# Optimization experiments

Hardware: AMD Instinct MI355X
Metric: run time of the kernel (lower is better)

The kernel has to match this reference:

```python
import jax, jax.numpy as jnp
import numpy as np

B, S, D, H, T = 16, 512, 512, 8, 8
DK = D // H
SCALE = float(1.0 / np.sqrt(DK))
EPS = 1e-5


def setup_inputs() -> dict:
    key = jax.random.key(0)
    ks = jax.random.split(key, 12)
    s = float(1.0 / np.sqrt(D))  # torch Linear default init scale
    u = lambda k, shp: jax.random.uniform(k, shp, jnp.float32, -s, s)
    return {
        "x": jax.random.normal(ks[0], (B, S, D), jnp.float32),
        "x_type": jax.random.randint(ks[1], (B, S), 0, T, jnp.int32),
        "mask": jax.random.randint(ks[2], (B, S, S), 0, 2, jnp.int32),
        "Wq": u(ks[3], (T, D, D)), "bq": u(ks[4], (T, D)),
        "Wk": u(ks[5], (T, D, D)), "bk": u(ks[6], (T, D)),
        "Wv": u(ks[7], (T, D, D)), "bv": u(ks[8], (T, D)),
        "Wa": u(ks[9], (T, D, D)), "ba": u(ks[10], (T, D)),
        "gamma": jnp.ones((T, D), jnp.float32),
        "beta": jnp.zeros((T, D), jnp.float32),
    }


def _typed_proj(xf, t, W, b):
    # per-node-type linear 'experts': compute all T projections, select by type id
    # xf: [N, D], W: [T, D, D], b: [T, D], t: [N] -> [N, D]
    all_p = jnp.einsum('nd,tdh->nth', xf, W) + b[None]  # [N, T, D]
    return jnp.take_along_axis(all_p, t[:, None, None], axis=1)[:, 0]


def reference(x, x_type, mask, Wq, bq, Wk, bk, Wv, bv, Wa, ba, gamma, beta):
    xf = x.reshape(-1, D)          # [N, D], N = B*S
    t = x_type.reshape(-1)         # [N]

    # heterogeneous Q/K/V dispatch
    q = _typed_proj(xf, t, Wq, bq).reshape(B, S, H, DK).transpose(0, 2, 1, 3)
    k = _typed_proj(xf, t, Wk, bk).reshape(B, S, H, DK).transpose(0, 2, 1, 3)
    v = _typed_proj(xf, t, Wv, bv).reshape(B, S, H, DK).transpose(0, 2, 1, 3)

    # scaled dot-product attention with boolean mask (mask==0 -> -1e9)
    scores = jnp.einsum('bhqd,bhkd->bhqk', q, k) * SCALE  # [B, H, S, S]
    scores = jnp.where(mask[:, None] == 0, jnp.float32(-1e9), scores)
    p = jax.nn.softmax(scores, axis=-1)
    att = jnp.einsum('bhqk,bhkd->bhqd', p, v)             # [B, H, S, DK]
    att = att.transpose(0, 2, 1, 3).reshape(-1, D)        # [N, D]

    # per-type output projection + residual + per-type LayerNorm
    a = _typed_proj(att, t, Wa, ba)
    h = a + xf
    mu = jnp.mean(h, axis=-1, keepdims=True)
    var = jnp.mean((h - mu) ** 2, axis=-1, keepdims=True)
    out = (h - mu) * jax.lax.rsqrt(var + EPS) * gamma[t] + beta[t]
    return out.reshape(B, S, D)
```

## Files before the change

kernel.cpp:

```cpp
#include <hip/hip_runtime.h>
#include <hip/hip_bf16.h>

typedef __attribute__((ext_vector_type(8))) short short8;
typedef __attribute__((ext_vector_type(4))) float f32x4;
typedef __attribute__((ext_vector_type(4))) unsigned short u16x4;
typedef unsigned short u16;
typedef unsigned int u32;
typedef unsigned long long u64;

#define NB 16
#define NS 512
#define ND 512
#define NH 8
#define NT 8
#define NDK 64
#define NN (NB*NS)
#define SCALE_LOG2E 0.18033688011112042f
#define BM 128
#define BN 128
#define BKK 64

__device__ __forceinline__ u16 f2bf(float f) {
    __hip_bfloat16 h = __float2bfloat16(f);
    return *reinterpret_cast<u16*>(&h);
}
__device__ __forceinline__ u32 pk2(float lo, float hi) {
    return (u32)f2bf(lo) | ((u32)f2bf(hi) << 16);
}

typedef const __attribute__((address_space(1))) void* gas_t;
typedef __attribute__((address_space(3))) void* las_t;

__device__ __forceinline__ void gload16(const void* gsrc, void* ldst) {
    __builtin_amdgcn_global_load_lds((gas_t)gsrc, (las_t)ldst, 16, 0, 0);
}

__global__ __launch_bounds__(256) void pre_all(
    const float* __restrict__ x, const int* __restrict__ xty, const int* __restrict__ mask,
    const float* __restrict__ Wq, const float* __restrict__ Wk,
    const float* __restrict__ Wv, const float* __restrict__ Wa,
    u16* __restrict__ xb,
    u16* __restrict__ Wqt, u16* __restrict__ Wkt, u16* __restrict__ Wvt, u16* __restrict__ Wat,
    u64* __restrict__ maskb, int* __restrict__ gcnt, int* __restrict__ scnt)
{
    __shared__ __align__(16) float tile[64][68];
    __shared__ int cnt[NT];
    int bid = blockIdx.x, tid = threadIdx.x;

    if (bid < 4096) {
        int i = bid * 256 + tid;
        float4 v = reinterpret_cast<const float4*>(x)[i];
        u16x4 o;
        o.x = f2bf(v.x); o.y = f2bf(v.y); o.z = f2bf(v.z); o.w = f2bf(v.w);
        reinterpret_cast<u16x4*>(xb)[i] = o;
    } else if (bid < 6144) {
        int wid = bid - 4096;
        int bx = wid & 7, by = (wid >> 3) & 7, bz = wid >> 6;
        int arr = bz >> 3, t = bz & 7;
        const float* W = (arr == 0 ? Wq : arr == 1 ? Wk : arr == 2 ? Wv : Wa) + ((size_t)t << 18);
        u16* O = (arr == 0 ? Wqt : arr == 1 ? Wkt : arr == 2 ? Wvt : Wat) + ((size_t)t << 18);
        int d0 = bx * 64, h0 = by * 64;
        int tx = tid & 15, ty = tid >> 4;
        #pragma unroll
        for (int i = 0; i < 4; ++i) {
            int r = ty + i * 16;
            float4 v = *reinterpret_cast<const float4*>(&W[(size_t)(d0 + r) * ND + h0 + tx * 4]);
            *reinterpret_cast<float4*>(&tile[r][tx * 4]) = v;
        }
        __syncthreads();
        #pragma unroll
        for (int i = 0; i < 4; ++i) {
            int r = ty + i * 16;
            u16x4 o;
            o.x = f2bf(tile[tx * 4 + 0][r]);
            o.y = f2bf(tile[tx * 4 + 1][r]);
            o.z = f2bf(tile[tx * 4 + 2][r]);
            o.w = f2bf(tile[tx * 4 + 3][r]);
            *reinterpret_cast<u16x4*>(&O[(size_t)(h0 + r) * ND + d0 + tx * 4]) = o;
        }
    } else if (bid < 7168) {
        int base = (bid - 6144) * 16;
        #pragma unroll
        for (int c = 0; c < 16; ++c) {
            int i = (base + c) * 256 + tid;
            int v = mask[i];
            u64 bal = __ballot(v != 0);
            if ((tid & 63) == 0) maskb[i >> 6] = bal;
        }
    } else {
        int s = bid - 7168;
        if (tid < NT) cnt[tid] = 0;
        __syncthreads();
        if (tid < 128) atomicAdd(&cnt[xty[s * 128 + tid]], 1);
        __syncthreads();
        if (tid < NT) {
            scnt[s * 8 + tid] = cnt[tid];
            atomicAdd(&gcnt[tid], cnt[tid]);
        }
    }
}

__global__ __launch_bounds__(256) void scatter_k(
    const int* __restrict__ xty, const int* __restrict__ gcnt, const int* __restrict__ scnt,
    int* __restrict__ perm, int* __restrict__ typeoff,
    int* __restrict__ tile_type, int* __restrict__ tile_row0, int* __restrict__ ntiles)
{
    __shared__ int base[NT];
    int s = blockIdx.x, tid = threadIdx.x;
    if (tid < NT) {
        int off = 0;
        for (int tt = 0; tt < tid; ++tt) off += gcnt[tt];
        base[tid] = off;
    }
    __syncthreads();
    {
        int t = tid & 7;
        for (int ss = tid >> 3; ss < s; ss += 32) atomicAdd(&base[t], scnt[ss * 8 + t]);
    }
    __syncthreads();
    if (tid < 128) {
        int n = s * 128 + tid;
        int t = xty[n];
        int p = atomicAdd(&base[t], 1);
        perm[p] = n;
    }
    if (s == 0 && tid == 0) {
        int acc = 0, nt = 0;
        for (int t = 0; t < NT; ++t) {
            typeoff[t] = acc;
            int c = gcnt[t];
            for (int r = 0; r < c; r += BM) { tile_type[nt] = t; tile_row0[nt] = acc + r; ++nt; }
            acc += c;
        }
        typeoff[NT] = acc;
        *ntiles = nt;
    }
}

__global__ __launch_bounds__(256) void qkv_gemm(
    const u16* __restrict__ xb,
    const u16* __restrict__ Wqt, const u16* __restrict__ Wkt, const u16* __restrict__ Wvt,
    const float* __restrict__ bq, const float* __restrict__ bk, const float* __restrict__ bv,
    const int* __restrict__ perm, const int* __restrict__ typeoff,
    const int* __restrict__ tile_type, const int* __restrict__ tile_row0, const int* __restrict__ ntiles,
    u16* __restrict__ qb, u16* __restrict__ kbf, u16* __restrict__ vb)
{
    int work = (blockIdx.x & 7) * 108 + (blockIdx.x >> 3);
    int tile = work / 12, pc = work % 12;
    if (tile >= *ntiles) return;
    int t = tile_type[tile];
    int row0 = tile_row0[tile];
    int rows = typeoff[t + 1] - row0; if (rows > BM) rows = BM;
    int proj = pc >> 2;
    int col0 = (pc & 3) * BN;
    const u16* W = (proj == 0 ? Wqt : proj == 1 ? Wkt : Wvt) + ((size_t)t << 18);
    const float* bias = (proj == 0 ? bq : proj == 1 ? bk : bv) + (t << 9);
    u16* outp = proj == 0 ? qb : proj == 1 ? kbf : vb;
    float qscale = proj == 0 ? SCALE_LOG2E : 1.f;

    __shared__ __align__(16) u16 smem[2][2][BM][BKK];
    __shared__ int stok[BM];
    auto As = smem[0]; auto Bs = smem[1];

    int tid = threadIdx.x;
    if (tid < BM) stok[tid] = perm[row0 + (tid < rows ? tid : 0)];
    __syncthreads();

    int lane = tid & 63, w = tid >> 6;
    int wr = w >> 1, wc = w & 1;
    int fr = lane & 15, g = lane >> 4;

    int lrow = lane >> 3;
    int schunk = (lane & 7) ^ lrow;
    int tokA[4];
    #pragma unroll
    for (int k = 0; k < 4; ++k) tokA[k] = stok[w * 32 + k * 8 + lrow];

    auto stage = [&](int buf, int k0) {
        #pragma unroll
        for (int k = 0; k < 4; ++k) {
            gload16(xb + (((size_t)tokA[k]) << 9) + k0 + schunk * 8, &As[buf][w * 32 + k * 8][0]);
            gload16(W + (((size_t)(col0 + w * 32 + k * 8 + lrow)) << 9) + k0 + schunk * 8,
                    &Bs[buf][w * 32 + k * 8][0]);
        }
    };

    f32x4 acc[4][4] = {};

    stage(0, 0);
    #pragma unroll
    for (int it = 0; it < 8; ++it) {
        int cur = it & 1;
        if (it < 7) {
            stage(cur ^ 1, (it + 1) * BKK);
            asm volatile("s_waitcnt vmcnt(8)" ::: "memory");
        } else {
            asm volatile("s_waitcnt vmcnt(0)" ::: "memory");
        }
        __builtin_amdgcn_s_barrier();

        const char* Ab = (const char*)As[cur];
        const char* Bb = (const char*)Bs[cur];
        #pragma unroll
        for (int ks = 0; ks < 2; ++ks) {
            short8 af[4], bfr[4];
            #pragma unroll
            for (int m = 0; m < 4; ++m) {
                int r = wr * 64 + m * 16 + fr;
                af[m] = *reinterpret_cast<const short8*>(Ab + r * 128 + (((ks * 4 + g) ^ (r & 7)) << 4));
            }
            #pragma unroll
            for (int n = 0; n < 4; ++n) {
                int r = wc * 64 + n * 16 + fr;
                bfr[n] = *reinterpret_cast<const short8*>(Bb + r * 128 + (((ks * 4 + g) ^ (r & 7)) << 4));
            }
            #pragma unroll
            for (int m = 0; m < 4; ++m)
                #pragma unroll
                for (int n = 0; n < 4; ++n)
                    acc[m][n] = __builtin_amdgcn_mfma_f32_16x16x32_bf16(af[m], bfr[n], acc[m][n], 0, 0, 0);
        }
        asm volatile("s_waitcnt lgkmcnt(0)" ::: "memory");
        __builtin_amdgcn_s_barrier();
    }

    u16 (*sT)[136] = reinterpret_cast<u16 (*)[136]>(&smem[0][0][0][0]);
    #pragma unroll
    for (int n = 0; n < 4; ++n) {
        int col = wc * 64 + n * 16 + fr;
        float bv_ = bias[col0 + col];
        #pragma unroll
        for (int m = 0; m < 4; ++m)
            #pragma unroll
            for (int i = 0; i < 4; ++i)
                sT[wr * 64 + m * 16 + g * 4 + i][col] = f2bf((acc[m][n][i] + bv_) * qscale);
    }
    __syncthreads();
    int r = tid >> 1, half = tid & 1;
    if (r < rows) {
        int tok = stok[r], b = tok >> 9, s = tok & 511;
        int h = (col0 >> 6) + half;
        u16* dst = outp + ((size_t)((b * NH + h) * NS + s) << 6);
        #pragma unroll
        for (int j = 0; j < 8; ++j)
            *reinterpret_cast<short8*>(dst + j * 8) =
                *reinterpret_cast<const short8*>(&sT[r][half * 64 + j * 8]);
    }
}

__global__ __launch_bounds__(256) void transp_v(const u16* __restrict__ vb, u16* __restrict__ vtb)
{
    int bh = blockIdx.y, s0 = blockIdx.x * 64;
    __shared__ __align__(16) u16 t[64][72];
    int tid = threadIdx.x;
    const u16* src = vb + ((size_t)bh << 15) + ((size_t)s0 << 6);
    #pragma unroll
    for (int it = 0; it < 2; ++it) {
        int idx = it * 256 + tid;
        int s = idx & 63, c = idx >> 6;
        short8 v = *reinterpret_cast<const short8*>(src + ((size_t)s << 6) + c * 8);
        #pragma unroll
        for (int j = 0; j < 8; ++j) t[c * 8 + j][s] = ((const u16*)&v)[j];
    }
    __syncthreads();
    u16* dst = vtb + ((size_t)bh << 15) + s0;
    #pragma unroll
    for (int it = 0; it < 2; ++it) {
        int idx = it * 256 + tid;
        int dk = idx >> 3, c = idx & 7;
        short8 v = *reinterpret_cast<const short8*>(&t[dk][c * 8]);
        *reinterpret_cast<short8*>(dst + (size_t)dk * NS + c * 8) = v;
    }
}

__global__ __launch_bounds__(256) void attn_mfma(
    const u16* __restrict__ qb, const u16* __restrict__ kbf, const u16* __restrict__ vtb,
    const u64* __restrict__ maskb, u16* __restrict__ attb)
{
    int work = (blockIdx.x & 7) * 128 + (blockIdx.x >> 3);
    int bh = work >> 3, jq = work & 7;
    int b = bh >> 3, h = bh & 7;
    int q0 = jq * 64;
    int tid = threadIdx.x, lane = tid & 63, w = tid >> 6;
    int ln15 = lane & 15, g = lane >> 4;

    __shared__ __align__(16) u16 sK[64 * 64];
    __shared__ __align__(16) u16 sVt[64 * 64];
    __shared__ __align__(16) u16 sP[4 * 16 * 68];

    const u16* Qg = qb + ((size_t)(bh * NS + q0 + w * 16 + ln15) << 6);
    short8 aq0 = *reinterpret_cast<const short8*>(Qg + g * 8);
    short8 aq1 = *reinterpret_cast<const short8*>(Qg + 32 + g * 8);

    const u16* Kg = kbf + ((size_t)bh << 15);
    const u16* Vtg = vtb + ((size_t)bh << 15);
    int srow = tid >> 3, schunk = tid & 7;

    const u64* Mq = maskb + ((size_t)((b << 9) + q0 + w * 16 + ln15)) * 8;
    float mrun = -3.0e38f, lrun = 0.f;
    f32x4 acc_o[4] = {};

    short8 kpre0 = *reinterpret_cast<const short8*>(Kg + ((size_t)srow << 6) + schunk * 8);
    short8 kpre1 = *reinterpret_cast<const short8*>(Kg + ((size_t)(srow + 32) << 6) + schunk * 8);
    short8 vpre0 = *reinterpret_cast<const short8*>(Vtg + (size_t)srow * NS + schunk * 8);
    short8 vpre1 = *reinterpret_cast<const short8*>(Vtg + (size_t)(srow + 32) * NS + schunk * 8);

    char* sPw = (char*)sP + w * 16 * 136;

    for (int j = 0; j < 8; ++j) {
        __syncthreads();
        {
            int r2 = srow + 32;
            *reinterpret_cast<short8*>((char*)sK  + srow * 128 + ((schunk * 16) ^ ((srow & 7) << 4))) = kpre0;
            *reinterpret_cast<short8*>((char*)sK  + r2   * 128 + ((schunk * 16) ^ ((r2   & 7) << 4))) = kpre1;
            *reinterpret_cast<short8*>((char*)sVt + srow * 128 + ((schunk * 16) ^ ((srow & 7) << 4))) = vpre0;
            *reinterpret_cast<short8*>((char*)sVt + r2   * 128 + ((schunk * 16) ^ ((r2   & 7) << 4))) = vpre1;
        }
        if (j < 7) {
            int j1 = j + 1;
            kpre0 = *reinterpret_cast<const short8*>(Kg + ((size_t)(j1 * 64 + srow) << 6) + schunk * 8);
            kpre1 = *reinterpret_cast<const short8*>(Kg + ((size_t)(j1 * 64 + srow + 32) << 6) + schunk * 8);
            vpre0 = *reinterpret_cast<const short8*>(Vtg + (size_t)srow * NS + j1 * 64 + schunk * 8);
            vpre1 = *reinterpret_cast<const short8*>(Vtg + (size_t)(srow + 32) * NS + j1 * 64 + schunk * 8);
        }
        __syncthreads();

        f32x4 accs[4] = {};
        __builtin_amdgcn_s_setprio(1);
        #pragma unroll
        for (int ks = 0; ks < 2; ++ks) {
            short8 bq_ = ks ? aq1 : aq0;
            #pragma unroll
            for (int n = 0; n < 4; ++n) {
                int row = n * 16 + ln15;
                short8 kfrag = *reinterpret_cast<const short8*>(
                    (char*)sK + row * 128 + (((ks * 64) + g * 16) ^ ((row & 7) << 4)));
                accs[n] = __builtin_amdgcn_mfma_f32_16x16x32_bf16(kfrag, bq_, accs[n], 0, 0, 0);
            }
        }
        __builtin_amdgcn_s_setprio(0);

        u64 mw = Mq[j];
        float sv[4][4];
        float mx = -3.0e38f;
        #pragma unroll
        for (int n = 0; n < 4; ++n) {
            u32 b4 = (u32)(mw >> (n * 16 + g * 4)) & 15u;
            #pragma unroll
            for (int r = 0; r < 4; ++r) {
                float s = (b4 >> r) & 1u ? accs[n][r] : -1.0e9f;
                sv[n][r] = s;
                mx = fmaxf(mx, s);
            }
        }
        mx = fmaxf(mx, __shfl_xor(mx, 16));
        mx = fmaxf(mx, __shfl_xor(mx, 32));

        if (__any(mx > mrun + 8.f)) {
            float nm = fmaxf(mrun, mx);
            float sc = exp2f(mrun - nm);
            mrun = nm;
            lrun *= sc;
            #pragma unroll
            for (int i = 0; i < 4; ++i) {
                float si = __shfl(sc, g * 4 + i);
                #pragma unroll
                for (int n2 = 0; n2 < 4; ++n2) acc_o[n2][i] *= si;
            }
        }

        float ps = 0.f;
        #pragma unroll
        for (int n = 0; n < 4; ++n) {
            float p0 = exp2f(sv[n][0] - mrun), p1 = exp2f(sv[n][1] - mrun);
            float p2 = exp2f(sv[n][2] - mrun), p3 = exp2f(sv[n][3] - mrun);
            ps += (p0 + p1) + (p2 + p3);
            *reinterpret_cast<u32*>(sPw + ln15 * 136 + n * 32 + g * 8 + 0) = pk2(p0, p1);
            *reinterpret_cast<u32*>(sPw + ln15 * 136 + n * 32 + g * 8 + 4) = pk2(p2, p3);
        }
        ps += __shfl_xor(ps, 16);
        ps += __shfl_xor(ps, 32);
        lrun += ps;

        __builtin_amdgcn_s_setprio(1);
        #pragma unroll
        for (int ks = 0; ks < 2; ++ks) {
            short8 ap = *reinterpret_cast<const short8*>(sPw + ln15 * 136 + ks * 64 + g * 16);
            #pragma unroll
            for (int n2 = 0; n2 < 4; ++n2) {
                int row = n2 * 16 + ln15;
                short8 vfrag = *reinterpret_cast<const short8*>(
                    (char*)sVt + row * 128 + (((ks * 64) + g * 16) ^ ((row & 7) << 4)));
                acc_o[n2] = __builtin_amdgcn_mfma_f32_16x16x32_bf16(ap, vfrag, acc_o[n2], 0, 0, 0);
            }
        }
        __builtin_amdgcn_s_setprio(0);
    }

    float linv = 1.f / lrun;
    #pragma unroll
    for (int i = 0; i < 4; ++i) {
        float li = __shfl(linv, g * 4 + i);
        int q = q0 + w * 16 + g * 4 + i;
        #pragma unroll
        for (int n2 = 0; n2 < 4; ++n2) {
            attb[((size_t)((b << 9) + q) << 9) + (h << 6) + n2 * 16 + ln15] =
                f2bf(acc_o[n2][i] * li);
        }
    }
}

__global__ __launch_bounds__(256) void out_gemm(
    const u16* __restrict__ attb, const u16* __restrict__ Wat, const float* __restrict__ ba,
    const int* __restrict__ perm, const int* __restrict__ typeoff,
    const int* __restrict__ tile_type, const int* __restrict__ tile_row0, const int* __restrict__ ntiles,
    const float* __restrict__ x, float* __restrict__ hbuf)
{
    int work = (blockIdx.x & 7) * 36 + (blockIdx.x >> 3);
    int tile = work >> 2;
    if (tile >= *ntiles) return;
    int t = tile_type[tile];
    int row0 = tile_row0[tile];
    int rows = typeoff[t + 1] - row0; if (rows > BM) rows = BM;
    int col0 = (work & 3) * BN;
    const u16* W = Wat + ((size_t)t << 18);
    const float* bias = ba + (t << 9);

    __shared__ __align__(16) u16 As[2][BM][BKK];
    __shared__ __align__(16) u16 Bs[2][BM][BKK];
    __shared__ int stok[BM];

    int tid = threadIdx.x;
    if (tid < BM) stok[tid] = perm[row0 + (tid < rows ? tid : 0)];
    __syncthreads();

    int lane = tid & 63, w = tid >> 6;
    int wr = w >> 1, wc = w & 1;
    int fr = lane & 15, g = lane >> 4;

    int lrow = lane >> 3;
    int schunk = (lane & 7) ^ lrow;
    int tokA[4];
    #pragma unroll
    for (int k = 0; k < 4; ++k) tokA[k] = stok[w * 32 + k * 8 + lrow];

    auto stage = [&](int buf, int k0) {
        #pragma unroll
        for (int k = 0; k < 4; ++k) {
            gload16(attb + (((size_t)tokA[k]) << 9) + k0 + schunk * 8, &As[buf][w * 32 + k * 8][0]);
            gload16(W + (((size_t)(col0 + w * 32 + k * 8 + lrow)) << 9) + k0 + schunk * 8,
                    &Bs[buf][w * 32 + k * 8][0]);
        }
    };

    f32x4 acc[4][4] = {};

    stage(0, 0);
    #pragma unroll
    for (int it = 0; it < 8; ++it) {
        int cur = it & 1;
        if (it < 7) {
            stage(cur ^ 1, (it + 1) * BKK);
            asm volatile("s_waitcnt vmcnt(8)" ::: "memory");
        } else {
            asm volatile("s_waitcnt vmcnt(0)" ::: "memory");
        }
        __builtin_amdgcn_s_barrier();

        const char* Ab = (const char*)As[cur];
        const char* Bb = (const char*)Bs[cur];
        #pragma unroll
        for (int ks = 0; ks < 2; ++ks) {
            short8 af[4], bfr[4];
            #pragma unroll
            for (int m = 0; m < 4; ++m) {
                int r = wr * 64 + m * 16 + fr;
                af[m] = *reinterpret_cast<const short8*>(Ab + r * 128 + (((ks * 4 + g) ^ (r & 7)) << 4));
            }
            #pragma unroll
            for (int n = 0; n < 4; ++n) {
                int r = wc * 64 + n * 16 + fr;
                bfr[n] = *reinterpret_cast<const short8*>(Bb + r * 128 + (((ks * 4 + g) ^ (r & 7)) << 4));
            }
            #pragma unroll
            for (int m = 0; m < 4; ++m)
                #pragma unroll
                for (int n = 0; n < 4; ++n)
                    acc[m][n] = __builtin_amdgcn_mfma_f32_16x16x32_bf16(af[m], bfr[n], acc[m][n], 0, 0, 0);
        }
        asm volatile("s_waitcnt lgkmcnt(0)" ::: "memory");
        __builtin_amdgcn_s_barrier();
    }

    int rbase = g << 2;
    #pragma unroll
    for (int n = 0; n < 4; ++n) {
        int c = col0 + wc * 64 + n * 16 + fr;
        float bv_ = bias[c];
        #pragma unroll
        for (int m = 0; m < 4; ++m) {
            #pragma unroll
            for (int i = 0; i < 4; ++i) {
                int r = wr * 64 + m * 16 + rbase + i;
                if (r < rows) {
                    int tok = stok[r];
                    size_t off = (size_t)tok * ND + c;
                    hbuf[off] = acc[m][n][i] + bv_ + x[off];
                }
            }
        }
    }
}

__global__ __launch_bounds__(256) void lnorm(
    const float* __restrict__ hbuf, const int* __restrict__ xty,
    const float* __restrict__ gamma, const float* __restrict__ beta, float* __restrict__ out)
{
    int row = blockIdx.x * 4 + (threadIdx.x >> 6);
    int lane = threadIdx.x & 63;
    const float4* h4 = reinterpret_cast<const float4*>(hbuf + (size_t)row * ND);
    float4 a = h4[lane * 2], b = h4[lane * 2 + 1];
    float sum = a.x + a.y + a.z + a.w + b.x + b.y + b.z + b.w;
    float sq = a.x * a.x + a.y * a.y + a.z * a.z + a.w * a.w
             + b.x * b.x + b.y * b.y + b.z * b.z + b.w * b.w;
    #pragma unroll
    for (int off = 32; off; off >>= 1) { sum += __shfl_xor(sum, off); sq += __shfl_xor(sq, off); }
    float mu = sum * (1.f / ND);
    float var = sq * (1.f / ND) - mu * mu;
    float is = rsqrtf(var + 1e-5f);
    int t = xty[row];
    const float4* g4 = reinterpret_cast<const float4*>(gamma + ((size_t)t << 9));
    const float4* be4 = reinterpret_cast<const float4*>(beta + ((size_t)t << 9));
    float4 g0 = g4[lane * 2], g1 = g4[lane * 2 + 1];
    float4 b0 = be4[lane * 2], b1 = be4[lane * 2 + 1];
    float4 o0, o1;
    o0.x = (a.x - mu) * is * g0.x + b0.x;
    o0.y = (a.y - mu) * is * g0.y + b0.y;
    o0.z = (a.z - mu) * is * g0.z + b0.z;
    o0.w = (a.w - mu) * is * g0.w + b0.w;
    o1.x = (b.x - mu) * is * g1.x + b1.x;
    o1.y = (b.y - mu) * is * g1.y + b1.y;
    o1.z = (b.z - mu) * is * g1.z + b1.z;
    o1.w = (b.w - mu) * is * g1.w + b1.w;
    float4* out4 = reinterpret_cast<float4*>(out + (size_t)row * ND);
    out4[lane * 2] = o0; out4[lane * 2 + 1] = o1;
}

extern "C" void kernel_launch(void* const* d_in, const int* in_sizes, int n_in,
                              void* d_out, int out_size, void* d_ws, size_t ws_size,
                              hipStream_t stream)
{
    const float* x     = (const float*)d_in[0];
    const int*   xty   = (const int*)d_in[1];
    const int*   mask  = (const int*)d_in[2];
    const float* Wq    = (const float*)d_in[3];
    const float* bq    = (const float*)d_in[4];
    const float* Wk    = (const float*)d_in[5];
    const float* bk    = (const float*)d_in[6];
    const float* Wv    = (const float*)d_in[7];
    const float* bv    = (const float*)d_in[8];
    const float* Wa    = (const float*)d_in[9];
    const float* ba    = (const float*)d_in[10];
    const float* gamma = (const float*)d_in[11];
    const float* beta  = (const float*)d_in[12];
    float* out = (float*)d_out;

    char* ws = (char*)d_ws;
    u16*   xb      = (u16*)(ws + 0);
    u16*   Wqt     = (u16*)(ws + 8388608);
    u16*   Wkt     = (u16*)(ws + 12582912);
    u16*   Wvt     = (u16*)(ws + 16777216);
    u16*   Wat     = (u16*)(ws + 20971520);
    u16*   qb      = (u16*)(ws + 25165824);
    u16*   kbf     = (u16*)(ws + 33554432);
    u16*   vb      = (u16*)(ws + 41943040);
    u16*   vtb     = (u16*)(ws + 50331648);
    u16*   attb    = (u16*)(ws + 58720256);
    float* hbuf    = (float*)(ws + 67108864);
    u64*   maskb   = (u64*)(ws + 83886080);
    int*   perm    = (int*)(ws + 84410368);
    int*   typeoff = (int*)(ws + 84443136);
    int*   ttile   = (int*)(ws + 84443200);
    int*   trow    = (int*)(ws + 84443776);
    int*   ntiles  = (int*)(ws + 84444352);
    int*   gcnt    = (int*)(ws + 84444416);
    int*   scnt    = (int*)(ws + 84444480);

    hipMemsetAsync(gcnt, 0, 32, stream);
    pre_all<<<dim3(7232), dim3(256), 0, stream>>>(x, xty, mask, Wq, Wk, Wv, Wa,
                                                  xb, Wqt, Wkt, Wvt, Wat, maskb, gcnt, scnt);
    scatter_k<<<dim3(64), dim3(256), 0, stream>>>(xty, gcnt, scnt, perm, typeoff, ttile, trow, ntiles);
    qkv_gemm<<<dim3(864), dim3(256), 0, stream>>>(xb, Wqt, Wkt, Wvt, bq, bk, bv,
                                                  perm, typeoff, ttile, trow, ntiles, qb, kbf, vb);
    transp_v<<<dim3(8, 128), dim3(256), 0, stream>>>(vb, vtb);
    attn_mfma<<<dim3(1024), dim3(256), 0, stream>>>(qb, kbf, vtb, maskb, attb);
    out_gemm<<<dim3(288), dim3(256), 0, stream>>>(attb, Wat, ba,
                                                  perm, typeoff, ttile, trow, ntiles, x, hbuf);
    lnorm<<<dim3(2048), dim3(256), 0, stream>>>(hbuf, xty, gamma, beta, out);
}
```

Baseline: 251.1 us.

## Remove memset, merge QKV column tiles per block, store residual buffer in bf16

The global type-count atomics and memset are dropped; scatter_k now sums the per-segment counts itself. qkv_gemm gives each block two consecutive 128-column tiles (half the blocks) so the gathered A rows are reused, with an epilogue between tiles. out_gemm reads the bf16 copy of x for the residual and writes the pre-norm sum as bf16, and lnorm reads bf16. This halves residual and intermediate traffic but rounds the residual sum to bf16, which adds error before LayerNorm.

Result: no change. 251.2 us (+0.0%).

```diff
diff --git a/kernel.cpp b/kernel.cpp
--- a/kernel.cpp
+++ b/kernel.cpp
@@ -24,6 +24,10 @@
     __hip_bfloat16 h = __float2bfloat16(f);
     return *reinterpret_cast<u16*>(&h);
 }
+__device__ __forceinline__ float bf2f(u16 b) {
+    u32 u = ((u32)b) << 16;
+    return *reinterpret_cast<float*>(&u);
+}
 __device__ __forceinline__ u32 pk2(float lo, float hi) {
     return (u32)f2bf(lo) | ((u32)f2bf(hi) << 16);
 }
@@ -41,7 +45,7 @@
     const float* __restrict__ Wv, const float* __restrict__ Wa,
     u16* __restrict__ xb,
     u16* __restrict__ Wqt, u16* __restrict__ Wkt, u16* __restrict__ Wvt, u16* __restrict__ Wat,
-    u64* __restrict__ maskb, int* __restrict__ gcnt, int* __restrict__ scnt)
+    u64* __restrict__ maskb, int* __restrict__ scnt)
 {
     __shared__ __align__(16) float tile[64][68];
     __shared__ int cnt[NT];
@@ -93,23 +97,26 @@
         __syncthreads();
         if (tid < 128) atomicAdd(&cnt[xty[s * 128 + tid]], 1);
         __syncthreads();
-        if (tid < NT) {
-            scnt[s * 8 + tid] = cnt[tid];
-            atomicAdd(&gcnt[tid], cnt[tid]);
-        }
+        if (tid < NT) scnt[s * 8 + tid] = cnt[tid];
     }
 }
 
 __global__ __launch_bounds__(256) void scatter_k(
-    const int* __restrict__ xty, const int* __restrict__ gcnt, const int* __restrict__ scnt,
+    const int* __restrict__ xty, const int* __restrict__ scnt,
     int* __restrict__ perm, int* __restrict__ typeoff,
     int* __restrict__ tile_type, int* __restrict__ tile_row0, int* __restrict__ ntiles)
 {
-    __shared__ int base[NT];
+    __shared__ int base[NT], tot[NT];
     int s = blockIdx.x, tid = threadIdx.x;
     if (tid < NT) {
+        int tt = 0;
+        for (int ss = 0; ss < 64; ++ss) tt += scnt[ss * 8 + tid];
+        tot[tid] = tt;
+    }
+    __syncthreads();
+    if (tid < NT) {
         int off = 0;
-        for (int tt = 0; tt < tid; ++tt) off += gcnt[tt];
+        for (int u = 0; u < tid; ++u) off += tot[u];
         base[tid] = off;
     }
     __syncthreads();
@@ -128,7 +135,7 @@
         int acc = 0, nt = 0;
         for (int t = 0; t < NT; ++t) {
             typeoff[t] = acc;
-            int c = gcnt[t];
+            int c = tot[t];
             for (int r = 0; r < c; r += BM) { tile_type[nt] = t; tile_row0[nt] = acc + r; ++nt; }
             acc += c;
         }
@@ -145,14 +152,15 @@
     const int* __restrict__ tile_type, const int* __restrict__ tile_row0, const int* __restrict__ ntiles,
     u16* __restrict__ qb, u16* __restrict__ kbf, u16* __restrict__ vb)
 {
-    int work = (blockIdx.x & 7) * 108 + (blockIdx.x >> 3);
-    int tile = work / 12, pc = work % 12;
+    int p = (blockIdx.x & 7) * 54 + (blockIdx.x >> 3);
+    int tile = p / 6;
     if (tile >= *ntiles) return;
+    int pairc = p % 6;
+    int proj = pairc >> 1;
+    int colbase = (pairc & 1) * 256;
     int t = tile_type[tile];
     int row0 = tile_row0[tile];
     int rows = typeoff[t + 1] - row0; if (rows > BM) rows = BM;
-    int proj = pc >> 2;
-    int col0 = (pc & 3) * BN;
     const u16* W = (proj == 0 ? Wqt : proj == 1 ? Wkt : Wvt) + ((size_t)t << 18);
     const float* bias = (proj == 0 ? bq : proj == 1 ? bk : bv) + (t << 9);
     u16* outp = proj == 0 ? qb : proj == 1 ? kbf : vb;
@@ -160,7 +168,6 @@
 
     __shared__ __align__(16) u16 smem[2][2][BM][BKK];
     __shared__ int stok[BM];
-    auto As = smem[0]; auto Bs = smem[1];
 
     int tid = threadIdx.x;
     if (tid < BM) stok[tid] = perm[row0 + (tid < rows ? tid : 0)];
@@ -169,38 +176,76 @@
     int lane = tid & 63, w = tid >> 6;
     int wr = w >> 1, wc = w & 1;
     int fr = lane & 15, g = lane >> 4;
-
     int lrow = lane >> 3;
     int schunk = (lane & 7) ^ lrow;
     int tokA[4];
     #pragma unroll
     for (int k = 0; k < 4; ++k) tokA[k] = stok[w * 32 + k * 8 + lrow];
 
-    auto stage = [&](int buf, int k0) {
+    auto stage = [&](int buf, int k0, int c0) {
         #pragma unroll
         for (int k = 0; k < 4; ++k) {
-            gload16(xb + (((size_t)tokA[k]) << 9) + k0 + schunk * 8, &As[buf][w * 32 + k * 8][0]);
-            gload16(W + (((size_t)(col0 + w * 32 + k * 8 + lrow)) << 9) + k0 + schunk * 8,
-                    &Bs[buf][w * 32 + k * 8][0]);
+            gload16(xb + (((size_t)tokA[k]) << 9) + k0 + schunk * 8, &smem[buf][0][w * 32 + k * 8][0]);
+            gload16(W + (((size_t)(c0 + w * 32 + k * 8 + lrow)) << 9) + k0 + schunk * 8,
+                    &smem[buf][1][w * 32 + k * 8][0]);
         }
     };
 
     f32x4 acc[4][4] = {};
 
-    stage(0, 0);
-    #pragma unroll
-    for (int it = 0; it < 8; ++it) {
-        int cur = it & 1;
-        if (it < 7) {
-            stage(cur ^ 1, (it + 1) * BKK);
+    auto epilogue = [&](int buf, int c0) {
+        u16* sT = &smem[buf][0][0][0];
+        #pragma unroll
+        for (int n = 0; n < 4; ++n) {
+            int wcol = wc * 64 + n * 16 + fr;
+            float bv_ = bias[c0 + wcol];
+            #pragma unroll
+            for (int m = 0; m < 4; ++m)
+                #pragma unroll
+                for (int i = 0; i < 4; ++i) {
+                    int r = wr * 64 + m * 16 + g * 4 + i;
+                    int ch = (wcol >> 3) ^ (r & 7);
+                    sT[r * 128 + ch * 8 + (wcol & 7)] = f2bf((acc[m][n][i] + bv_) * qscale);
+                }
+        }
+        asm volatile("s_waitcnt lgkmcnt(0)" ::: "memory");
+        __builtin_amdgcn_s_barrier();
+        int r = tid >> 1, h2 = tid & 1;
+        if (r < rows) {
+            int tok = stok[r], b = tok >> 9, s = tok & 511;
+            int h = (c0 >> 6) + h2;
+            u16* dst = outp + ((size_t)((b * NH + h) * NS + s) << 6);
+            #pragma unroll
+            for (int j2 = 0; j2 < 8; ++j2) {
+                int ch = (h2 * 8 + j2) ^ (r & 7);
+                *reinterpret_cast<short8*>(dst + j2 * 8) =
+                    *reinterpret_cast<const short8*>(&sT[r * 128 + ch * 8]);
+            }
+        }
+        asm volatile("s_waitcnt lgkmcnt(0)" ::: "memory");
+        __builtin_amdgcn_s_barrier();
+        #pragma unroll
+        for (int m = 0; m < 4; ++m)
+            #pragma unroll
+            for (int n = 0; n < 4; ++n)
+                acc[m][n] = (f32x4){0.f, 0.f, 0.f, 0.f};
+    };
+
+    stage(0, 0, colbase);
+    #pragma unroll
+    for (int j = 0; j < 16; ++j) {
+        int cur = j & 1;
+        if (j < 15) {
+            int jn = j + 1;
+            stage(cur ^ 1, (jn & 7) * BKK, colbase + (jn >> 3) * BN);
             asm volatile("s_waitcnt vmcnt(8)" ::: "memory");
         } else {
             asm volatile("s_waitcnt vmcnt(0)" ::: "memory");
         }
         __builtin_amdgcn_s_barrier();
 
-        const char* Ab = (const char*)As[cur];
-        const char* Bb = (const char*)Bs[cur];
+        const char* Ab = (const char*)&smem[cur][0][0][0];
+        const char* Bb = (const char*)&smem[cur][1][0][0];
         #pragma unroll
         for (int ks = 0; ks < 2; ++ks) {
             short8 af[4], bfr[4];
@@ -222,30 +267,10 @@
         }
         asm volatile("s_waitcnt lgkmcnt(0)" ::: "memory");
         __builtin_amdgcn_s_barrier();
-    }
-
-    u16 (*sT)[136] = reinterpret_cast<u16 (*)[136]>(&smem[0][0][0][0]);
-    #pragma unroll
-    for (int n = 0; n < 4; ++n) {
-        int col = wc * 64 + n * 16 + fr;
-        float bv_ = bias[col0 + col];
-        #pragma unroll
-        for (int m = 0; m < 4; ++m)
-            #pragma unroll
-            for (int i = 0; i < 4; ++i)
-                sT[wr * 64 + m * 16 + g * 4 + i][col] = f2bf((acc[m][n][i] + bv_) * qscale);
-    }
-    __syncthreads();
-    int r = tid >> 1, half = tid & 1;
-    if (r < rows) {
-        int tok = stok[r], b = tok >> 9, s = tok & 511;
-        int h = (col0 >> 6) + half;
-        u16* dst = outp + ((size_t)((b * NH + h) * NS + s) << 6);
-        #pragma unroll
-        for (int j = 0; j < 8; ++j)
-            *reinterpret_cast<short8*>(dst + j * 8) =
-                *reinterpret_cast<const short8*>(&sT[r][half * 64 + j * 8]);
-    }
+
+        if (j == 7) epilogue(1, colbase);
+    }
+    epilogue(1, colbase + BN);
 }
 
 __global__ __launch_bounds__(256) void transp_v(const u16* __restrict__ vb, u16* __restrict__ vtb)
@@ -414,7 +439,7 @@
     const u16* __restrict__ attb, const u16* __restrict__ Wat, const float* __restrict__ ba,
     const int* __restrict__ perm, const int* __restrict__ typeoff,
     const int* __restrict__ tile_type, const int* __restrict__ tile_row0, const int* __restrict__ ntiles,
-    const float* __restrict__ x, float* __restrict__ hbuf)
+    const u16* __restrict__ xb, u16* __restrict__ hbuf)
 {
     int work = (blockIdx.x & 7) * 36 + (blockIdx.x >> 3);
     int tile = work >> 2;
@@ -505,7 +530,7 @@
                 if (r < rows) {
                     int tok = stok[r];
                     size_t off = (size_t)tok * ND + c;
-                    hbuf[off] = acc[m][n][i] + bv_ + x[off];
+                    hbuf[off] = f2bf(acc[m][n][i] + bv_ + bf2f(xb[off]));
                 }
             }
         }
@@ -513,37 +538,41 @@
 }
 
 __global__ __launch_bounds__(256) void lnorm(
-    const float* __restrict__ hbuf, const int* __restrict__ xty,
+    const u16* __restrict__ hbuf, const int* __restrict__ xty,
     const float* __restrict__ gamma, const float* __restrict__ beta, float* __restrict__ out)
 {
     int row = blockIdx.x * 4 + (threadIdx.x >> 6);
     int lane = threadIdx.x & 63;
-    const float4* h4 = reinterpret_cast<const float4*>(hbuf + (size_t)row * ND);
-    float4 a = h4[lane * 2], b = h4[lane * 2 + 1];
-    float sum = a.x + a.y + a.z + a.w + b.x + b.y + b.z + b.w;
-    float sq = a.x * a.x + a.y * a.y + a.z * a.z + a.w * a.w
-             + b.x * b.x + b.y * b.y + b.z * b.z + b.w * b.w;
+    short8 v = *reinterpret_cast<const short8*>(hbuf + (size_t)row * ND + lane * 8);
+    float f[8];
+    float sum = 0.f, sq = 0.f;
+    #pragma unroll
+    for (int k = 0; k < 8; ++k) {
+        f[k] = bf2f(((const u16*)&v)[k]);
+        sum += f[k];
+        sq += f[k] * f[k];
+    }
     #pragma unroll
     for (int off = 32; off; off >>= 1) { sum += __shfl_xor(sum, off); sq += __shfl_xor(sq, off); }
     float mu = sum * (1.f / ND);
     float var = sq * (1.f / ND) - mu * mu;
     float is = rsqrtf(var + 1e-5f);
     int t = xty[row];
-    const float4* g4 = reinterpret_cast<const float4*>(gamma + ((size_t)t << 9));
-    const float4* be4 = reinterpret_cast<const float4*>(beta + ((size_t)t << 9));
-    float4 g0 = g4[lane * 2], g1 = g4[lane * 2 + 1];
-    float4 b0 = be4[lane * 2], b1 = be4[lane * 2 + 1];
+    const float4* g4 = reinterpret_cast<const float4*>(gamma + ((size_t)t << 9) + lane * 8);
+    const float4* b4 = reinterpret_cast<const float4*>(beta + ((size_t)t << 9) + lane * 8);
+    float4 g0 = g4[0], g1 = g4[1];
+    float4 b0 = b4[0], b1 = b4[1];
     float4 o0, o1;
-    o0.x = (a.x - mu) * is * g0.x + b0.x;
-    o0.y = (a.y - mu) * is * g0.y + b0.y;
-    o0.z = (a.z - mu) * is * g0.z + b0.z;
-    o0.w = (a.w - mu) * is * g0.w + b0.w;
-    o1.x = (b.x - mu) * is * g1.x + b1.x;
-    o1.y = (b.y - mu) * is * g1.y + b1.y;
-    o1.z = (b.z - mu) * is * g1.z + b1.z;
-    o1.w = (b.w - mu) * is * g1.w + b1.w;
-    float4* out4 = reinterpret_cast<float4*>(out + (size_t)row * ND);
-    out4[lane * 2] = o0; out4[lane * 2 + 1] = o1;
+    o0.x = (f[0] - mu) * is * g0.x + b0.x;
+    o0.y = (f[1] - mu) * is * g0.y + b0.y;
+    o0.z = (f[2] - mu) * is * g0.z + b0.z;
+    o0.w = (f[3] - mu) * is * g0.w + b0.w;
+    o1.x = (f[4] - mu) * is * g1.x + b1.x;
+    o1.y = (f[5] - mu) * is * g1.y + b1.y;
+    o1.z = (f[6] - mu) * is * g1.z + b1.z;
+    o1.w = (f[7] - mu) * is * g1.w + b1.w;
+    float4* out4 = reinterpret_cast<float4*>(out + (size_t)row * ND + lane * 8);
+    out4[0] = o0; out4[1] = o1;
 }
 
 extern "C" void kernel_launch(void* const* d_in, const int* in_sizes, int n_in,
@@ -576,25 +605,23 @@
     u16*   vb      = (u16*)(ws + 41943040);
     u16*   vtb     = (u16*)(ws + 50331648);
     u16*   attb    = (u16*)(ws + 58720256);
-    float* hbuf    = (float*)(ws + 67108864);
+    u16*   hbuf    = (u16*)(ws + 67108864);
     u64*   maskb   = (u64*)(ws + 83886080);
     int*   perm    = (int*)(ws + 84410368);
     int*   typeoff = (int*)(ws + 84443136);
     int*   ttile   = (int*)(ws + 84443200);
     int*   trow    = (int*)(ws + 84443776);
     int*   ntiles  = (int*)(ws + 84444352);
-    int*   gcnt    = (int*)(ws + 84444416);
     int*   scnt    = (int*)(ws + 84444480);
 
-    hipMemsetAsync(gcnt, 0, 32, stream);
     pre_all<<<dim3(7232), dim3(256), 0, stream>>>(x, xty, mask, Wq, Wk, Wv, Wa,
-                                                  xb, Wqt, Wkt, Wvt, Wat, maskb, gcnt, scnt);
-    scatter_k<<<dim3(64), dim3(256), 0, stream>>>(xty, gcnt, scnt, perm, typeoff, ttile, trow, ntiles);
-    qkv_gemm<<<dim3(864), dim3(256), 0, stream>>>(xb, Wqt, Wkt, Wvt, bq, bk, bv,
+                                                  xb, Wqt, Wkt, Wvt, Wat, maskb, scnt);
+    scatter_k<<<dim3(64), dim3(256), 0, stream>>>(xty, scnt, perm, typeoff, ttile, trow, ntiles);
+    qkv_gemm<<<dim3(432), dim3(256), 0, stream>>>(xb, Wqt, Wkt, Wvt, bq, bk, bv,
                                                   perm, typeoff, ttile, trow, ntiles, qb, kbf, vb);
     transp_v<<<dim3(8, 128), dim3(256), 0, stream>>>(vb, vtb);
     attn_mfma<<<dim3(1024), dim3(256), 0, stream>>>(qb, kbf, vtb, maskb, attb);
     out_gemm<<<dim3(288), dim3(256), 0, stream>>>(attb, Wat, ba,
-                                                  perm, typeoff, ttile, trow, ntiles, x, hbuf);
+                                                  perm, typeoff, ttile, trow, ntiles, xb, hbuf);
     lnorm<<<dim3(2048), dim3(256), 0, stream>>>(hbuf, xty, gamma, beta, out);
 }
```
